# Performance work log

Measured on AMD Instinct MI355X. Metric: run time of the kernel, lower is better.

The kernel has to match this reference:

```python
import jax, jax.numpy as jnp
import numpy as np

NUM_CODES = 1024
CODE_DIM = 256
COMMITMENT_COST = 0.25
B, T = 32, 1024


def setup_inputs() -> dict:
    key = jax.random.key(0)
    k1, k2 = jax.random.split(key)
    latents = jax.random.normal(k1, (B, CODE_DIM, T), dtype=jnp.float32)
    # faithful to nn.Embedding init uniform_(-1/num_codes, 1/num_codes)
    codebook = jax.random.uniform(k2, (NUM_CODES, CODE_DIM), dtype=jnp.float32,
                                  minval=-1.0 / NUM_CODES, maxval=1.0 / NUM_CODES)
    return {"latents": latents, "codebook": codebook}


def reference(latents, codebook):
    # latents: [B, D, T], codebook: [K, D]
    b, d, t = latents.shape
    flat = jnp.transpose(latents, (0, 2, 1)).reshape(-1, d)  # [B*T, D]
    distances = (jnp.sum(flat * flat, axis=1, keepdims=True)
                 - 2.0 * flat @ codebook.T
                 + jnp.sum(codebook * codebook, axis=1))  # [B*T, K]
    indices = jnp.argmin(distances, axis=1)  # [B*T]
    quantized = codebook[indices].reshape(b, t, d).transpose(0, 2, 1)  # [B, D, T]
    codebook_loss = jnp.mean((quantized - jax.lax.stop_gradient(latents)) ** 2)
    commitment_loss = jnp.mean((jax.lax.stop_gradient(quantized) - latents) ** 2)
    loss = codebook_loss + COMMITMENT_COST * commitment_loss
    # straight-through estimator
    quantized_st = latents + jax.lax.stop_gradient(quantized - latents)
    return quantized_st, loss, indices.reshape(b, t)
```

## Files before the change

kernel.cpp:

```cpp
#include <hip/hip_runtime.h>
#include <math.h>

#define Dd 256
#define Tt 1024
#define Bb 32
#define Kk 1024
#define NROWS (Bb*Tt)
#define OUTQ  (Bb*Dd*Tt)
#define KP   512
#define SLACK 4e-4f
#define LIST_CAP 458752u
#define CANDB_CAP 1024u

typedef __bf16 b16x8 __attribute__((ext_vector_type(8)));
typedef float  f32x4 __attribute__((ext_vector_type(4)));

#define OFF_LOSS  0
#define OFF_GCNT  8
#define OFF_W2    256
#define OFF_X2    8192
#define OFF_IDX   139264
#define OFF_PACK  270336
#define OFF_GMIN  532480
#define OFF_RMING 663552
#define OFF_LIST  1712128
#define OFF_BT    5382144
#define OFF_X     6430720
#define OFF_A     39985152
#define MIN_WS    (OFF_A + (size_t)NROWS*KP*2)

__global__ void vq_w2(const float* __restrict__ cb, float* __restrict__ w2f) {
#pragma clang fp contract(off)
    const int k = blockIdx.x * 256 + threadIdx.x;
    if (k >= Kk) return;
    const float* w = cb + (size_t)k * Dd;
    float h[2];
    for (int half = 0; half < 2; ++half) {
        const float* p = w + half * 128;
        float r[8];
        for (int j = 0; j < 8; ++j) { float v = p[j]; r[j] = v * v; }
        for (int m = 1; m < 16; ++m)
            for (int j = 0; j < 8; ++j) { float v = p[m*8 + j]; r[j] += v * v; }
        h[half] = ((r[0]+r[1]) + (r[2]+r[3])) + ((r[4]+r[5]) + (r[6]+r[7]));
    }
    w2f[k] = h[0] + h[1];
}

__global__ void vq_prep_bt(const float* __restrict__ cb, __bf16* __restrict__ BT) {
    const int c = blockIdx.x, t = threadIdx.x;
    float v = cb[(size_t)c*Dd + t];
    __bf16 hi = (__bf16)v;
    BT[(size_t)c*KP + t]       = hi;
    BT[(size_t)c*KP + 256 + t] = hi;
}

__global__ void vq_prep_a(const float* __restrict__ lat, float* __restrict__ X,
                          __bf16* __restrict__ A) {
    __shared__ float tl[64][65];
    const int tid = threadIdx.x;
    const int rowbase = blockIdx.x * 64;
    const int b = rowbase >> 10, t0 = rowbase & 1023;
    const int d0 = blockIdx.y * 64;
    const int tt = tid & 63, sub = tid >> 6;
#pragma unroll
    for (int it = 0; it < 16; ++it) {
        int d = it*4 + sub;
        tl[d][tt] = lat[((size_t)(b*Dd + d0 + d))*Tt + t0 + tt];
    }
    __syncthreads();
    const int dd = tid & 63;
#pragma unroll
    for (int it = 0; it < 16; ++it) {
        int t = it*4 + sub;
        float v = tl[dd][t];
        int grow = rowbase + t;
        X[(size_t)grow*Dd + d0 + dd] = v;
        __bf16 hi = (__bf16)v;
        __bf16 lo = (__bf16)(v - (float)hi);
        size_t ab = (size_t)grow*KP + d0 + dd;
        A[ab]       = hi;
        A[ab + 256] = lo;
    }
}

__global__ __launch_bounds__(256) void vq_x2(const float* __restrict__ X,
                                             float* __restrict__ x2f) {
    __shared__ float xrow[4][256];
    const int tid = threadIdx.x;
    const int wv = tid >> 6, l = tid & 63;
    const int row = blockIdx.x * 4 + wv;

    const float4* xg = (const float4*)(X + (size_t)row * Dd);
    *(float4*)&xrow[wv][l*4] = xg[l];
    __syncthreads();

    float s = 0.0f;
    if (l < 16) {
#pragma clang fp contract(off)
        const int h = l >> 3, j = l & 7;
        float v = xrow[wv][h*128 + j];
        float r8 = v * v;
        for (int m = 1; m < 16; ++m) {
            v = xrow[wv][h*128 + m*8 + j];
            r8 += v * v;
        }
        s = r8;
    }
    s += __shfl_xor(s, 1, 64);
    s += __shfl_xor(s, 2, 64);
    s += __shfl_xor(s, 4, 64);
    s += __shfl_xor(s, 8, 64);
    if (l == 0) x2f[row] = s;
}

__global__ __launch_bounds__(256) void vq_gemm(const __bf16* __restrict__ A,
                                               const __bf16* __restrict__ BT,
                                               const float* __restrict__ w2f,
                                               unsigned* __restrict__ gcnt,
                                               uint2* __restrict__ list,
                                               float* __restrict__ rming) {
    __shared__ __bf16 As[128][72];
    __shared__ __bf16 Bs[128][72];
    __shared__ float  rminS[128][2];
    __shared__ unsigned nCand;
    __shared__ unsigned baseS;
    __shared__ unsigned candRC[CANDB_CAP];
    __shared__ float    candF [CANDB_CAP];

    const int tid = threadIdx.x;
    const int bm = blockIdx.x, bn = blockIdx.y;
    const int l = tid & 63, wv = tid >> 6;
    const int wm = (wv & 1) * 64, wn = (wv >> 1) * 64;
    const int m16 = l & 15, quad = l >> 4;

    if (tid == 0) nCand = 0u;

    f32x4 acc[4][4];
#pragma unroll
    for (int i = 0; i < 4; ++i)
#pragma unroll
        for (int j = 0; j < 4; ++j) acc[i][j] = (f32x4){0.f,0.f,0.f,0.f};

    const int sr = tid >> 3;
    const int sk = (tid & 7) * 8;

    for (int kt = 0; kt < 8; ++kt) {
        const int k0 = kt * 64;
#pragma unroll
        for (int p = 0; p < 4; ++p) {
            int r = sr + p*32;
            *(uint4*)&As[r][sk] = *(const uint4*)&A [(size_t)(bm*128 + r)*KP + k0 + sk];
            *(uint4*)&Bs[r][sk] = *(const uint4*)&BT[(size_t)(bn*128 + r)*KP + k0 + sk];
        }
        __syncthreads();
#pragma unroll
        for (int ks = 0; ks < 64; ks += 32) {
            b16x8 a[4], b[4];
#pragma unroll
            for (int i = 0; i < 4; ++i) a[i] = *(const b16x8*)&As[wm + 16*i + m16][ks + quad*8];
#pragma unroll
            for (int j = 0; j < 4; ++j) b[j] = *(const b16x8*)&Bs[wn + 16*j + m16][ks + quad*8];
#pragma unroll
            for (int i = 0; i < 4; ++i)
#pragma unroll
                for (int j = 0; j < 4; ++j)
                    acc[i][j] = __builtin_amdgcn_mfma_f32_16x16x32_bf16(a[i], b[j], acc[i][j], 0, 0, 0);
        }
        __syncthreads();
    }

    float w2n[4];
#pragma unroll
    for (int j = 0; j < 4; ++j) w2n[j] = w2f[bn*128 + wn + 16*j + m16];

    float vmin[4][4];
#pragma unroll
    for (int i = 0; i < 4; ++i)
#pragma unroll
        for (int g = 0; g < 4; ++g) {
            float v = w2n[0] - 2.0f * acc[i][0][g];
#pragma unroll
            for (int j = 1; j < 4; ++j)
                v = fminf(v, w2n[j] - 2.0f * acc[i][j][g]);
#pragma unroll
            for (int off = 1; off <= 8; off <<= 1)
                v = fminf(v, __shfl_xor(v, off, 64));
            vmin[i][g] = v;
        }
    if (m16 == 0) {
#pragma unroll
        for (int i = 0; i < 4; ++i)
#pragma unroll
            for (int g = 0; g < 4; ++g)
                rminS[wm + 16*i + quad*4 + g][wn >> 6] = vmin[i][g];
    }
    __syncthreads();
    if (tid < 128)
        rming[((size_t)(bm*128 + tid))*8 + bn] = fminf(rminS[tid][0], rminS[tid][1]);
#pragma unroll
    for (int i = 0; i < 4; ++i)
#pragma unroll
        for (int g = 0; g < 4; ++g) {
            const int rloc = wm + 16*i + quad*4 + g;
            const float thr = fminf(rminS[rloc][0], rminS[rloc][1]) + SLACK;
#pragma unroll
            for (int j = 0; j < 4; ++j) {
                float f = w2n[j] - 2.0f * acc[i][j][g];
                if (f <= thr) {
                    unsigned slot = atomicAdd(&nCand, 1u);
                    if (slot < CANDB_CAP) {
                        candRC[slot] = ((unsigned)(bm*128 + rloc) << 10)
                                     | (unsigned)(bn*128 + wn + 16*j + m16);
                        candF[slot]  = f;
                    }
                }
            }
        }
    __syncthreads();
    unsigned nc = nCand; if (nc > CANDB_CAP) nc = CANDB_CAP;
    if (tid == 0) baseS = atomicAdd(gcnt, nc);
    __syncthreads();
    const unsigned base = baseS;
    for (unsigned i = tid; i < nc; i += 256) {
        unsigned dst = base + i;
        if (dst < LIST_CAP) {
            uint2 e; e.x = candRC[i]; e.y = __float_as_uint(candF[i]);
            list[dst] = e;
        }
    }
}

__global__ __launch_bounds__(256) void vq_gmin(const float* __restrict__ rming,
                                               float* __restrict__ gmin) {
    const int row = blockIdx.x * 256 + threadIdx.x;
    const float4* p = (const float4*)(rming + (size_t)row * 8);
    float4 a = p[0], b = p[1];
    float m = fminf(fminf(fminf(a.x, a.y), fminf(a.z, a.w)),
                    fminf(fminf(b.x, b.y), fminf(b.z, b.w)));
    gmin[row] = m + SLACK;
}

__global__ __launch_bounds__(256) void vq_rescore(const float* __restrict__ X,
                                                  const float* __restrict__ cb,
                                                  const float* __restrict__ w2f,
                                                  const float* __restrict__ x2f,
                                                  const float* __restrict__ gmin,
                                                  const unsigned* __restrict__ gcnt,
                                                  const uint2* __restrict__ list,
                                                  unsigned long long* __restrict__ pack) {
    unsigned n = *gcnt; if (n > LIST_CAP) n = LIST_CAP;
    const unsigned stride = gridDim.x * 256u;
    for (unsigned i = blockIdx.x * 256u + threadIdx.x; i < n; i += stride) {
        const uint2 e = list[i];
        const int row = (int)(e.x >> 10);
        const int c   = (int)(e.x & 1023u);
        if (__uint_as_float(e.y) > gmin[row]) continue;

        const float4* wq = (const float4*)(cb + (size_t)c * Dd);
        const float4* xq = (const float4*)(X + (size_t)row * Dd);
        float acc = 0.0f;
#pragma unroll 8
        for (int m = 0; m < 64; ++m) {
            float4 xa = xq[m], wa = wq[m];
            acc = __builtin_fmaf(xa.x, wa.x, acc);
            acc = __builtin_fmaf(xa.y, wa.y, acc);
            acc = __builtin_fmaf(xa.z, wa.z, acc);
            acc = __builtin_fmaf(xa.w, wa.w, acc);
        }
        float t2 = x2f[row] - 2.0f * acc;
        float dv = t2 + w2f[c];
        unsigned long long pk = ((unsigned long long)__float_as_uint(dv) << 32)
                              | (unsigned long long)(unsigned)c;
        atomicMin(&pack[row], pk);
    }
}

__global__ __launch_bounds__(256) void vq_pick(const unsigned long long* __restrict__ pack,
                                               int* __restrict__ idx,
                                               double* __restrict__ loss_acc) {
    __shared__ double wsum[4];
    const int tid = threadIdx.x;
    const int row = blockIdx.x * 256 + tid;
    const unsigned long long pk = pack[row];
    idx[row] = (int)(pk & 0xFFFFFFFFull);
    double d = (double)__uint_as_float((unsigned)(pk >> 32));
    for (int off = 32; off; off >>= 1) d += __shfl_xor(d, off, 64);
    if ((tid & 63) == 0) wsum[tid >> 6] = d;
    __syncthreads();
    if (tid == 0) atomicAdd(loss_acc, wsum[0] + wsum[1] + wsum[2] + wsum[3]);
}

typedef float float8_t __attribute__((ext_vector_type(8)));
__global__ __launch_bounds__(512) void vq_main(const float* __restrict__ latents,
                                               const float* __restrict__ cb,
                                               const float* __restrict__ w2f,
                                               int* __restrict__ idx,
                                               double* __restrict__ loss_acc) {
    __shared__ float  xs[Dd*64];
    __shared__ float  x2f[64];
    __shared__ float  bsd[8*64];
    __shared__ int    bci[8*64];
    __shared__ double red[64];
    const int tid = threadIdx.x;
    const int rr  = tid & 63;
    const int dg  = tid >> 6;
    const int blk = blockIdx.x;
    const int bb  = blk >> 4;
    const int t0  = (blk & 15) << 6;
    const float* lat = latents + (size_t)bb * Dd * Tt + t0;
    for (int d = dg; d < Dd; d += 8) xs[d*64 + rr] = lat[(size_t)d * Tt + rr];
    __syncthreads();
    if (tid < 64) {
#pragma clang fp contract(off)
        float h[2];
        for (int half = 0; half < 2; ++half) {
            float r[8];
            for (int j = 0; j < 8; ++j) { float v = xs[(half*128 + j)*64 + tid]; r[j] = v*v; }
            for (int m = 1; m < 16; ++m)
                for (int j = 0; j < 8; ++j) { float v = xs[(half*128 + m*8 + j)*64 + tid]; r[j] += v*v; }
            h[half] = ((r[0]+r[1]) + (r[2]+r[3])) + ((r[4]+r[5]) + (r[6]+r[7]));
        }
        x2f[tid] = h[0] + h[1];
    }
    __syncthreads();
    const int slab = __builtin_amdgcn_readfirstlane(tid >> 6);
    const int lane = tid & 63;
    const float x2r = x2f[lane];
    const float* wq = cb + (size_t)slab * 128 * Dd;
    float best = 3.4e38f; int bestc = 0;
    for (int cg = 0; cg < 16; ++cg) {
        const int c0 = cg * 8;
        float acc[8];
#pragma unroll
        for (int g = 0; g < 8; ++g) acc[g] = 0.0f;
        for (int kc = 0; kc < 32; ++kc) {
            float8_t w8[8];
#pragma unroll
            for (int g = 0; g < 8; ++g) w8[g] = *(const float8_t*)(wq + (size_t)(c0+g)*Dd + kc*8);
            float xk[8];
#pragma unroll
            for (int j = 0; j < 8; ++j) xk[j] = xs[(kc*8 + j)*64 + lane];
#pragma unroll
            for (int g = 0; g < 8; ++g)
#pragma unroll
                for (int j = 0; j < 8; ++j) acc[g] = __builtin_fmaf(xk[j], w8[g][j], acc[g]);
        }
#pragma unroll
        for (int g = 0; g < 8; ++g) {
            float t2 = x2r - 2.0f * acc[g];
            float dvv = t2 + w2f[slab*128 + c0 + g];
            if (dvv < best) { best = dvv; bestc = slab*128 + c0 + g; }
        }
    }
    bsd[slab*64 + lane] = best; bci[slab*64 + lane] = bestc;
    __syncthreads();
    if (tid < 64) {
        float b0 = bsd[tid]; int ci = bci[tid];
#pragma unroll
        for (int s = 1; s < 8; ++s) { float b1 = bsd[s*64 + tid]; if (b1 < b0) { b0 = b1; ci = bci[s*64 + tid]; } }
        idx[blk*64 + tid] = ci; red[tid] = (double)b0;
    }
    __syncthreads();
    if (tid == 0) { double s = 0.0; for (int i = 0; i < 64; ++i) s += red[i]; atomicAdd(loss_acc, s); }
}

__global__ void vq_gather(const float* __restrict__ cb,
                          const int* __restrict__ idx,
                          float* __restrict__ out) {
    const size_t g = (size_t)blockIdx.x * 256 + threadIdx.x;
    const int t  = (int)(g & 1023);
    const int d4 = (int)((g >> 10) & 63);
    const int b  = (int)(g >> 16);
    const int i  = idx[b*Tt + t];
    const float4 w4 = *(const float4*)(cb + (size_t)i*Dd + d4*4);
    float* o = out + ((size_t)(b*Dd + d4*4)) * Tt + t;
    o[0]    = w4.x;
    o[Tt]   = w4.y;
    o[2*Tt] = w4.z;
    o[3*Tt] = w4.w;
}

__global__ void vq_finalize(const int* __restrict__ idx,
                            const double* __restrict__ loss_acc,
                            float* __restrict__ out) {
    const int r = blockIdx.x * 256 + threadIdx.x;
    if (r < NROWS) out[OUTQ + 1 + r] = (float)idx[r];
    if (r == 0)    out[OUTQ] = (float)(1.25 * loss_acc[0] / (double)OUTQ);
}

extern "C" void kernel_launch(void* const* d_in, const int* in_sizes, int n_in,
                              void* d_out, int out_size, void* d_ws, size_t ws_size,
                              hipStream_t stream) {
    const float* latents = (const float*)d_in[0];
    const float* cb      = (const float*)d_in[1];
    float* out = (float*)d_out;
    char*  ws  = (char*)d_ws;

    double* loss = (double*)(ws + OFF_LOSS);
    float*  w2f  = (float*)(ws + OFF_W2);
    int*    idx  = (int*)(ws + OFF_IDX);

    hipMemsetAsync(ws, 0, 16, stream);
    vq_w2<<<4, 256, 0, stream>>>(cb, w2f);

    if (ws_size >= (size_t)MIN_WS) {
        unsigned*           gcnt  = (unsigned*)(ws + OFF_GCNT);
        float*              x2f   = (float*)(ws + OFF_X2);
        unsigned long long* pack  = (unsigned long long*)(ws + OFF_PACK);
        float*              gmin  = (float*)(ws + OFF_GMIN);
        float*              rming = (float*)(ws + OFF_RMING);
        uint2*              list  = (uint2*)(ws + OFF_LIST);
        __bf16*             BT    = (__bf16*)(ws + OFF_BT);
        float*              X     = (float*)(ws + OFF_X);
        __bf16*             A     = (__bf16*)(ws + OFF_A);

        hipMemsetAsync(pack, 0xFF, sizeof(unsigned long long) * NROWS, stream);
        vq_prep_bt<<<Kk, 256, 0, stream>>>(cb, BT);
        vq_prep_a<<<dim3(NROWS/64, 4), 256, 0, stream>>>(latents, X, A);
        vq_x2<<<NROWS/4, 256, 0, stream>>>(X, x2f);
        vq_gemm<<<dim3(NROWS/128, 8), 256, 0, stream>>>(A, BT, w2f, gcnt, list, rming);
        vq_gmin<<<NROWS/256, 256, 0, stream>>>(rming, gmin);
        vq_rescore<<<1024, 256, 0, stream>>>(X, cb, w2f, x2f, gmin, gcnt, list, pack);
        vq_pick<<<NROWS/256, 256, 0, stream>>>(pack, idx, loss);
    } else {
        vq_main<<<NROWS/64, 512, 0, stream>>>(latents, cb, w2f, idx, loss);
    }

    vq_gather<<<(Bb*(Dd/4)*Tt)/256, 256, 0, stream>>>(cb, idx, out);
    vq_finalize<<<(NROWS + 255)/256, 256, 0, stream>>>(idx, loss, out);
}
```

Baseline: 236.3 us.

## Load GEMM tiles directly to LDS with XOR swizzle and alias shared memory

The bf16 GEMM tile loads now use global_load_lds, which sends 16-byte chunks straight into LDS without staging them in registers. The padded 72-wide layout is replaced by an unpadded 64-wide layout with an XOR swizzle to avoid bank conflicts. The epilogue buffers (rminS, candidate lists, counters) alias the same 32KB shared buffer, which shrinks LDS use and may allow more blocks per CU. The cost is a more fragile address mapping, and correctness depends on the barrier before the epilogue reuses the tile memory.

New measurement: 233.3 us. Within noise of the previous version (-1.2%).

```diff
diff --git a/kernel.cpp b/kernel.cpp
--- a/kernel.cpp
+++ b/kernel.cpp
@@ -29,6 +29,12 @@
 #define OFF_A     39985152
 #define MIN_WS    (OFF_A + (size_t)NROWS*KP*2)
 
+__device__ __forceinline__ void gload16(const void* g, void* l) {
+    __builtin_amdgcn_global_load_lds(
+        (const __attribute__((address_space(1))) void*)g,
+        (__attribute__((address_space(3))) void*)l, 16, 0, 0);
+}
+
 __global__ void vq_w2(const float* __restrict__ cb, float* __restrict__ w2f) {
 #pragma clang fp contract(off)
     const int k = blockIdx.x * 256 + threadIdx.x;
@@ -119,13 +125,14 @@
                                                unsigned* __restrict__ gcnt,
                                                uint2* __restrict__ list,
                                                float* __restrict__ rming) {
-    __shared__ __bf16 As[128][72];
-    __shared__ __bf16 Bs[128][72];
-    __shared__ float  rminS[128][2];
-    __shared__ unsigned nCand;
-    __shared__ unsigned baseS;
-    __shared__ unsigned candRC[CANDB_CAP];
-    __shared__ float    candF [CANDB_CAP];
+    __shared__ __align__(16) char smem[32768];
+    __bf16* As = (__bf16*)smem;
+    __bf16* Bs = (__bf16*)(smem + 16384);
+    float (*rminS)[2] = (float(*)[2])smem;
+    unsigned* nCand   = (unsigned*)(smem + 1024);
+    unsigned* baseS   = (unsigned*)(smem + 1032);
+    unsigned* candRC  = (unsigned*)(smem + 2048);
+    float*    candF   = (float*)(smem + 6144);
 
     const int tid = threadIdx.x;
     const int bm = blockIdx.x, bn = blockIdx.y;
@@ -133,33 +140,40 @@
     const int wm = (wv & 1) * 64, wn = (wv >> 1) * 64;
     const int m16 = l & 15, quad = l >> 4;
 
-    if (tid == 0) nCand = 0u;
-
     f32x4 acc[4][4];
 #pragma unroll
     for (int i = 0; i < 4; ++i)
 #pragma unroll
         for (int j = 0; j < 4; ++j) acc[i][j] = (f32x4){0.f,0.f,0.f,0.f};
 
-    const int sr = tid >> 3;
-    const int sk = (tid & 7) * 8;
+    const int r8  = l >> 3;
+    const int c8  = l & 7;
+    const int csw = ((c8 ^ r8) * 8);
+    const int sw  = m16 & 7;
 
     for (int kt = 0; kt < 8; ++kt) {
         const int k0 = kt * 64;
 #pragma unroll
         for (int p = 0; p < 4; ++p) {
-            int r = sr + p*32;
-            *(uint4*)&As[r][sk] = *(const uint4*)&A [(size_t)(bm*128 + r)*KP + k0 + sk];
-            *(uint4*)&Bs[r][sk] = *(const uint4*)&BT[(size_t)(bn*128 + r)*KP + k0 + sk];
+            const int R0 = wv*32 + p*8;
+            gload16(&A [(size_t)(bm*128 + R0 + r8)*KP + k0 + csw], &As[R0*64]);
+            gload16(&BT[(size_t)(bn*128 + R0 + r8)*KP + k0 + csw], &Bs[R0*64]);
         }
         __syncthreads();
 #pragma unroll
         for (int ks = 0; ks < 64; ks += 32) {
+            const int k8 = ks >> 3;
             b16x8 a[4], b[4];
 #pragma unroll
-            for (int i = 0; i < 4; ++i) a[i] = *(const b16x8*)&As[wm + 16*i + m16][ks + quad*8];
-#pragma unroll
-            for (int j = 0; j < 4; ++j) b[j] = *(const b16x8*)&Bs[wn + 16*j + m16][ks + quad*8];
+            for (int i = 0; i < 4; ++i) {
+                const int row = wm + 16*i + m16;
+                a[i] = *(const b16x8*)((const char*)As + row*128 + (((k8 + quad) ^ sw) * 16));
+            }
+#pragma unroll
+            for (int j = 0; j < 4; ++j) {
+                const int row = wn + 16*j + m16;
+                b[j] = *(const b16x8*)((const char*)Bs + row*128 + (((k8 + quad) ^ sw) * 16));
+            }
 #pragma unroll
             for (int i = 0; i < 4; ++i)
 #pragma unroll
@@ -194,6 +208,7 @@
             for (int g = 0; g < 4; ++g)
                 rminS[wm + 16*i + quad*4 + g][wn >> 6] = vmin[i][g];
     }
+    if (tid == 0) *nCand = 0u;
     __syncthreads();
     if (tid < 128)
         rming[((size_t)(bm*128 + tid))*8 + bn] = fminf(rminS[tid][0], rminS[tid][1]);
@@ -207,7 +222,7 @@
             for (int j = 0; j < 4; ++j) {
                 float f = w2n[j] - 2.0f * acc[i][j][g];
                 if (f <= thr) {
-                    unsigned slot = atomicAdd(&nCand, 1u);
+                    unsigned slot = atomicAdd(nCand, 1u);
                     if (slot < CANDB_CAP) {
                         candRC[slot] = ((unsigned)(bm*128 + rloc) << 10)
                                      | (unsigned)(bn*128 + wn + 16*j + m16);
@@ -217,10 +232,10 @@
             }
         }
     __syncthreads();
-    unsigned nc = nCand; if (nc > CANDB_CAP) nc = CANDB_CAP;
-    if (tid == 0) baseS = atomicAdd(gcnt, nc);
-    __syncthreads();
-    const unsigned base = baseS;
+    unsigned nc = *nCand; if (nc > CANDB_CAP) nc = CANDB_CAP;
+    if (tid == 0) *baseS = atomicAdd(gcnt, nc);
+    __syncthreads();
+    const unsigned base = *baseS;
     for (unsigned i = tid; i < nc; i += 256) {
         unsigned dst = base + i;
         if (dst < LIST_CAP) {
```
